# Performance work log

Measured on AMD Instinct MI355X. Metric: run time of the kernel, lower is better.

## Reference

```python
import jax, jax.numpy as jnp
import numpy as np

B, T = 128, 2048
N_IN, N_H, N_OUT = 16, 128, 5
I_DECAY, V_DECAY = 1024, 128          # Loihi 12-bit decay constants
ALPHA_I = (4096 - I_DECAY) / 4096.0   # current decay multiplier
ALPHA_V = (4096 - V_DECAY) / 4096.0   # voltage decay multiplier
W_SCALE = 64.0                        # Loihi synaptic weight scaling (1 << 6)
THETA = 1 * 64.0                      # vThMant * (1 << 6)
SCALE_RHO, TAU_RHO = 1.0, 1.0
SG_TAU = TAU_RHO * THETA              # surrogate-gradient width


@jax.custom_vjp
def spike_fn(x):
    # Heaviside spike with SLAYER exponential surrogate gradient
    return (x >= 0).astype(x.dtype)

def _spike_fwd(x):
    return spike_fn(x), x

def _spike_bwd(x, g):
    return (g * (SCALE_RHO / SG_TAU) * jnp.exp(-jnp.abs(x) / SG_TAU),)

spike_fn.defvjp(_spike_fwd, _spike_bwd)


def weight_norm(v, g):
    # torch weight_norm with dim=0: per-output-row normalization
    return g[:, None] * v / jnp.linalg.norm(v, axis=1, keepdims=True)


def loihi_spikes(z):
    # z: (B, O, T) synaptic input. Sequential Loihi CUBA integrate-and-fire.
    zt = jnp.transpose(z, (2, 0, 1))  # (T, B, O)

    def step(carry, zin):
        u, v = carry
        u = ALPHA_I * u + zin          # synaptic current
        v = ALPHA_V * v + u            # membrane voltage
        s = spike_fn(v - THETA)
        v = v * (1.0 - s)              # reset-to-zero on spike
        return (u, v), s

    init = (jnp.zeros(zt.shape[1:], zt.dtype), jnp.zeros(zt.shape[1:], zt.dtype))
    _, s = jax.lax.scan(step, init, zt)
    return jnp.transpose(s, (1, 2, 0))  # (B, O, T)


def delay_shift1(x):
    # shift spikes one timestep later (slayer.delayShift(spike, 1))
    return jnp.concatenate([jnp.zeros_like(x[..., :1]), x[..., :-1]], axis=-1)


def axon_delay(x, d):
    # per-channel fractional delay via linear interpolation; x: (B,C,T), d: (C,)
    Tn = x.shape[-1]
    d0 = jnp.floor(d)
    f = (d - d0)[None, :, None]
    d0i = d0.astype(jnp.int32)
    t = jnp.arange(Tn, dtype=jnp.int32)

    def gather(shift):
        idx = t[None, :] - shift[:, None]          # (C, T)
        g = jnp.take_along_axis(
            x, jnp.broadcast_to(jnp.clip(idx, 0, Tn - 1)[None], x.shape), axis=-1)
        return jnp.where((idx >= 0)[None], g, 0.0)

    return (1.0 - f) * gather(d0i) + f * gather(d0i + 1)


def setup_inputs() -> dict:
    key = jax.random.key(0)
    ks = jax.random.split(key, 8)
    spike = (jax.random.uniform(ks[0], (B, N_IN, T)) < 0.1).astype(jnp.float32)
    fc1_v = jax.random.normal(ks[1], (N_H, N_IN), jnp.float32)
    fc2_v = jax.random.normal(ks[2], (N_H, N_H), jnp.float32)
    fc3_v = jax.random.normal(ks[3], (N_OUT, N_H), jnp.float32)
    # weight_norm init: g = ||v|| so W == v initially
    fc1_g = jnp.linalg.norm(fc1_v, axis=1)
    fc2_g = jnp.linalg.norm(fc2_v, axis=1)
    fc3_g = jnp.linalg.norm(fc3_v, axis=1)
    delay1 = jax.random.uniform(ks[4], (N_H,), jnp.float32) * 10.0
    delay2 = jax.random.uniform(ks[5], (N_H,), jnp.float32) * 10.0
    return {"spike": spike, "fc1_v": fc1_v, "fc1_g": fc1_g, "fc2_v": fc2_v,
            "fc2_g": fc2_g, "fc3_v": fc3_v, "fc3_g": fc3_g,
            "delay1": delay1, "delay2": delay2}


def reference(spike, fc1_v, fc1_g, fc2_v, fc2_g, fc3_v, fc3_g, delay1, delay2):
    x = spike.reshape(spike.shape[0], -1, spike.shape[-1])  # (B, 16, T)
    counts = []

    s = loihi_spikes(W_SCALE * jnp.einsum('oc,bct->bot', weight_norm(fc1_v, fc1_g), x))
    s = delay_shift1(s)
    counts.append(jnp.sum(s))
    s = axon_delay(s, delay1)

    s = loihi_spikes(W_SCALE * jnp.einsum('oc,bct->bot', weight_norm(fc2_v, fc2_g), s))
    s = delay_shift1(s)
    counts.append(jnp.sum(s))
    s = axon_delay(s, delay2)

    s = loihi_spikes(W_SCALE * jnp.einsum('oc,bct->bot', weight_norm(fc3_v, fc3_g), s))
    s = delay_shift1(s)
    counts.append(jnp.sum(s))

    return s, jnp.stack(counts).reshape(1, 3)
```

## Files before the change

### kernel.cpp

```cpp
#include <hip/hip_runtime.h>
#include <cstdint>

#define B_    128
#define T_    2048
#define NIN_  16
#define NH_   128
#define NOUT_ 5

#define ALPHA_I_ 0.75f
#define ALPHA_V_ 0.96875f
#define THETA_   64.0f

#define NCHUNK_ 8
#define CHT_    256
#define WARM_   96

typedef short bf16x8 __attribute__((ext_vector_type(8)));
typedef float f32x16 __attribute__((ext_vector_type(16)));

__device__ __forceinline__ float mulrn(float a, float b) { return __fmul_rn(a, b); }
__device__ __forceinline__ float addrn(float a, float b) { return __fadd_rn(a, b); }

__device__ __forceinline__ uint16_t f2bf(float x) {
  uint32_t u = __float_as_uint(x);
  return (uint16_t)((u + 0x7FFFu + ((u >> 16) & 1u)) >> 16);
}

__device__ __forceinline__ bf16x8 expand8(const uint2* __restrict__ lut, uint32_t byt) {
  uint2 lo = lut[byt & 15u];
  uint2 h  = lut[byt >> 4];
  union { uint32_t w[4]; bf16x8 f; } r;
  r.w[0] = lo.x; r.w[1] = lo.y; r.w[2] = h.x; r.w[3] = h.y;
  return r.f;
}

__device__ __forceinline__ void lut_init(uint2* s_lut, int tid) {
  if (tid < 16) {
    uint32_t w0 = ((tid & 1) ? 0x3F80u : 0u) | ((tid & 2) ? 0x3F800000u : 0u);
    uint32_t w1 = ((tid & 4) ? 0x3F80u : 0u) | ((tid & 8) ? 0x3F800000u : 0u);
    s_lut[tid] = make_uint2(w0, w1);
  }
}

__global__ __launch_bounds__(1024) void prep_kernel(
    const float* __restrict__ fc1_v, const float* __restrict__ fc1_g,
    const float* __restrict__ fc2_v, const float* __restrict__ fc2_g,
    const float* __restrict__ fc3_v, const float* __restrict__ fc3_g,
    const float* __restrict__ delay1, const float* __restrict__ delay2,
    uint16_t* __restrict__ w1swz, uint16_t* __restrict__ wswz,
    float* __restrict__ w3T, float4* __restrict__ efo1, float4* __restrict__ efo2,
    float* __restrict__ counts) {
  __shared__ float s_n1[NH_], s_n2[NH_], s_n3[8], s_g2[NH_];
  int tid = threadIdx.x;
  {
    int o = tid >> 3, sub = tid & 7;
    float ss = 0.f;
    for (int c = sub; c < NIN_; c += 8) { float v = fc1_v[o * NIN_ + c]; ss = __fmaf_rn(v, v, ss); }
    ss += __shfl_down(ss, 4, 64); ss += __shfl_down(ss, 2, 64); ss += __shfl_down(ss, 1, 64);
    if (sub == 0) s_n1[o] = sqrtf(ss);
    float ss2 = 0.f;
    for (int c = sub; c < NH_; c += 8) { float v = fc2_v[o * NH_ + c]; ss2 = __fmaf_rn(v, v, ss2); }
    ss2 += __shfl_down(ss2, 4, 64); ss2 += __shfl_down(ss2, 2, 64); ss2 += __shfl_down(ss2, 1, 64);
    if (sub == 0) s_n2[o] = sqrtf(ss2);
  }
  if (tid < NOUT_ * 8) {
    int o = tid >> 3, sub = tid & 7;
    float ss = 0.f;
    for (int c = sub; c < NH_; c += 8) { float v = fc3_v[o * NH_ + c]; ss = __fmaf_rn(v, v, ss); }
    ss += __shfl_down(ss, 4, 64); ss += __shfl_down(ss, 2, 64); ss += __shfl_down(ss, 1, 64);
    if (sub == 0) s_n3[o] = sqrtf(ss);
  }
  if (tid < NH_) s_g2[tid] = fc2_g[tid];
  if (tid < 3) counts[tid] = 0.f;
  __syncthreads();

  if (tid < NH_) {
    float d1 = delay1[tid];
    float fl = floorf(d1);
    float f = __fsub_rn(d1, fl);
    efo1[tid] = make_float4(__int_as_float((int)fl + 1), f, __fsub_rn(1.0f, f), 0.f);
    float d2 = delay2[tid];
    float fl2 = floorf(d2);
    float f2v = __fsub_rn(d2, fl2);
    efo2[tid] = make_float4(__int_as_float((int)fl2 + 1), f2v, __fsub_rn(1.0f, f2v), 0.f);
    w3T[tid * 8 + 5] = f2v;
    w3T[tid * 8 + 6] = __fsub_rn(1.0f, f2v);
    w3T[tid * 8 + 7] = 0.f;
  }
  for (int i = tid; i < NH_ * NIN_; i += 1024) {
    int o = i >> 4, c = i & 15;
    float wv = 64.0f * __fdiv_rn(mulrn(fc1_g[o], fc1_v[i]), s_n1[o]);
    int mt = o >> 5, lane = (o & 31) + 32 * ((c >> 3) & 1), j = c & 7;
    w1swz[(mt * 64 + lane) * 8 + j] = f2bf(wv);
  }
  for (int i = tid; i < NH_ * NH_; i += 1024) {
    int o = i >> 7, c = i & 127;
    float wv = 64.0f * __fdiv_rn(mulrn(s_g2[o], fc2_v[i]), s_n2[o]);
    float d1 = delay1[c];
    float f = __fsub_rn(d1, floorf(d1));
    int lane = (o & 31) + 32 * ((c >> 3) & 1);
    int ks = c >> 4, j = c & 7, mt = o >> 5;
    wswz[((size_t)((0 * 4 + mt) * 8 + ks) * 64 + lane) * 8 + j] = f2bf(__fmul_rn(wv, f));
    wswz[((size_t)((1 * 4 + mt) * 8 + ks) * 64 + lane) * 8 + j] =
        f2bf(__fmul_rn(wv, __fsub_rn(1.0f, f)));
  }
  for (int i = tid; i < NOUT_ * NH_; i += 1024) {
    int o = i / NH_, c = i & 127;
    float wv = 64.0f * __fdiv_rn(mulrn(fc3_g[o], fc3_v[i]), s_n3[o]);
    w3T[c * 8 + o] = wv;
  }
}

__global__ __launch_bounds__(256) void pack_kernel(const float* __restrict__ spike,
                                                   uint16_t* __restrict__ Xb) {
  int gw = blockIdx.x * 4 + (threadIdx.x >> 6);
  int lane = threadIdx.x & 63;
  int b = gw >> 5;
  int t = (gw & 31) * 64 + lane;
  const float* sp = spike + (size_t)b * NIN_ * T_ + t;
  uint32_t mask = 0;
#pragma unroll
  for (int c = 0; c < NIN_; c++) {
    unsigned long long bal = __ballot(sp[(size_t)c * T_] != 0.f);
    mask |= (uint32_t)((bal >> lane) & 1ull) << c;
  }
  Xb[(size_t)b * T_ + t] = (uint16_t)mask;
}

#define GATHER_AND_SCAN(aA, aB, hi, u, v, m)                               \
  {                                                                        \
    float evenQ[16], oddQ[16];                                             \
    _Pragma("unroll") for (int r = 0; r < 16; r++) {                       \
      float tmp = hi ? aA[r] : aB[r];                                      \
      float rcv = __shfl_xor(tmp, 32, 64);                                 \
      evenQ[r] = hi ? rcv : aA[r];                                         \
      oddQ[r] = hi ? aB[r] : rcv;                                          \
    }                                                                      \
    m = 0u;                                                                \
    _Pragma("unroll") for (int t = 0; t < 32; t++) {                       \
      int q = t >> 2;                                                      \
      int base = 4 * (q >> 1) + (t & 3);                                   \
      float z = (q & 1) ? oddQ[base] : evenQ[base];                        \
      u = addrn(mulrn(ALPHA_I_, u), z);                                    \
      v = addrn(mulrn(ALPHA_V_, v), u);                                    \
      bool sbit = (v >= THETA_);                                           \
      v = sbit ? 0.f : v;                                                  \
      m |= sbit ? (1u << t) : 0u;                                          \
    }                                                                      \
  }

#define EMIT_PT(m, m_prev, e_o, ptw, chwstart)                             \
  {                                                                        \
    uint32_t sm = (uint32_t)((((uint64_t)(m) << 32) | (m_prev)) >> (32 - (e_o))); \
    uint32_t myword = 0u;                                                  \
    _Pragma("unroll") for (int j = 0; j < 32; j++) {                       \
      unsigned long long bal_ = __ballot(((sm >> j) & 1u) != 0u);          \
      uint32_t w_ = hi ? (uint32_t)(bal_ >> 32) : (uint32_t)bal_;          \
      myword = (tl == j) ? w_ : myword;                                    \
    }                                                                      \
    ptw[(size_t)(1 + (chwstart) + tl) * 4 + (pair * 2 + hi)] = myword;     \
  }

__global__ __launch_bounds__(128, 2) void fused_layer1(const uint16_t* __restrict__ Xb,
                                                       const uint16_t* __restrict__ w1swz,
                                                       const float4* __restrict__ efo,
                                                       uint32_t* __restrict__ PT1,
                                                       float* __restrict__ cnt) {
  __shared__ uint2 s_lut[16];
  int tid = threadIdx.x;
  int pair = tid >> 6, lane = tid & 63;
  int hi = lane >> 5, tl = lane & 31;
  int ci = blockIdx.x, b = blockIdx.y;
  lut_init(s_lut, tid);
  const bf16x8* w1v = (const bf16x8*)w1swz;
  bf16x8 wA = w1v[(pair * 2 + 0) * 64 + lane];
  bf16x8 wB = w1v[(pair * 2 + 1) * 64 + lane];
  int e_o = __float_as_int(efo[tid].x);
  __syncthreads();

  int wch = (ci == 0) ? 0 : (WARM_ / 32);
  int nch = CHT_ / 32 + wch;
  int chbase0 = ci * CHT_ - wch * 32;
  const uint16_t* xb = Xb + (size_t)b * T_;
  uint32_t* ptw = PT1 + (size_t)b * (T_ + 1) * 4;

  float u = 0.f, v = 0.f, csum = 0.f;
  uint32_t m_prev = 0u;
  uint32_t x = xb[chbase0 + tl];
  for (int g = 0; g < nch; g++) {
    uint32_t xn = (g + 1 < nch) ? (uint32_t)xb[chbase0 + (g + 1) * 32 + tl] : 0u;
    uint32_t byt = (x >> (8 * hi)) & 0xFFu;
    bf16x8 e = expand8(s_lut, byt);
    f32x16 aA, aB;
#pragma unroll
    for (int r = 0; r < 16; r++) { aA[r] = 0.f; aB[r] = 0.f; }
    aA = __builtin_amdgcn_mfma_f32_32x32x16_bf16(e, wA, aA, 0, 0, 0);
    aB = __builtin_amdgcn_mfma_f32_32x32x16_bf16(e, wB, aB, 0, 0, 0);
    uint32_t m;
    GATHER_AND_SCAN(aA, aB, hi, u, v, m);
    if (g >= wch) {
      int chwstart = chbase0 + g * 32;
      EMIT_PT(m, m_prev, e_o, ptw, chwstart);
      int gw = chwstart >> 5;
      int pc = __popc(m);
      if (gw == 63) pc -= (int)(m >> 31);
      csum += (float)pc;
    }
    m_prev = m;
    x = xn;
  }
  if (ci == 0 && tid < 4) ptw[tid] = 0u;
  for (int off = 32; off; off >>= 1) csum += __shfl_down(csum, off, 64);
  if (lane == 0) atomicAdd(cnt, csum);
}

__global__ __launch_bounds__(128, 2) void fused_layer2(const uint32_t* __restrict__ PT1,
                                                       const uint16_t* __restrict__ wswz,
                                                       const float4* __restrict__ efo,
                                                       uint32_t* __restrict__ PT2,
                                                       float* __restrict__ cnt) {
  __shared__ uint2 s_lut[16];
  int tid = threadIdx.x;
  int pair = tid >> 6, lane = tid & 63;
  int hi = lane >> 5, tl = lane & 31;
  int ci = blockIdx.x, b = blockIdx.y;
  lut_init(s_lut, tid);
  const bf16x8* wsv = (const bf16x8*)wswz;
  int mtA = pair * 2, mtB = pair * 2 + 1;
  bf16x8 wfA[8], woA[8], wfB[8], woB[8];
#pragma unroll
  for (int ks = 0; ks < 8; ks++) {
    wfA[ks] = wsv[((size_t)((0 * 4 + mtA) * 8 + ks) * 64) + lane];
    woA[ks] = wsv[((size_t)((1 * 4 + mtA) * 8 + ks) * 64) + lane];
    wfB[ks] = wsv[((size_t)((0 * 4 + mtB) * 8 + ks) * 64) + lane];
    woB[ks] = wsv[((size_t)((1 * 4 + mtB) * 8 + ks) * 64) + lane];
  }
  int e_o = __float_as_int(efo[tid].x);
  __syncthreads();

  int wch = (ci == 0) ? 0 : (WARM_ / 32);
  int nch = CHT_ / 32 + wch;
  int chbase0 = ci * CHT_ - wch * 32;
  const uint4* pt = (const uint4*)PT1 + (size_t)b * (T_ + 1);
  uint32_t* ptw = PT2 + (size_t)b * (T_ + 1) * 4;

  float u = 0.f, v = 0.f, csum = 0.f;
  uint32_t m_prev = 0u;
  uint4 R0 = pt[chbase0 + tl];
  uint4 R1 = pt[chbase0 + tl + 1];
  for (int g = 0; g < nch; g++) {
    uint4 R0n = R0, R1n = R1;
    if (g + 1 < nch) {
      R0n = pt[chbase0 + (g + 1) * 32 + tl];
      R1n = pt[chbase0 + (g + 1) * 32 + tl + 1];
    }
    uint32_t r0w[4] = {R0.x, R0.y, R0.z, R0.w};
    uint32_t r1w[4] = {R1.x, R1.y, R1.z, R1.w};
    f32x16 aA, aB;
#pragma unroll
    for (int r = 0; r < 16; r++) { aA[r] = 0.f; aB[r] = 0.f; }
#pragma unroll
    for (int ks = 0; ks < 8; ks++) {
      int sh = 16 * (ks & 1) + 8 * hi;
      uint32_t b0 = (r0w[ks >> 1] >> sh) & 0xFFu;
      uint32_t b1 = (r1w[ks >> 1] >> sh) & 0xFFu;
      bf16x8 e0 = expand8(s_lut, b0);
      bf16x8 e1 = expand8(s_lut, b1);
      aA = __builtin_amdgcn_mfma_f32_32x32x16_bf16(e0, wfA[ks], aA, 0, 0, 0);
      aA = __builtin_amdgcn_mfma_f32_32x32x16_bf16(e1, woA[ks], aA, 0, 0, 0);
      aB = __builtin_amdgcn_mfma_f32_32x32x16_bf16(e0, wfB[ks], aB, 0, 0, 0);
      aB = __builtin_amdgcn_mfma_f32_32x32x16_bf16(e1, woB[ks], aB, 0, 0, 0);
    }
    uint32_t m;
    GATHER_AND_SCAN(aA, aB, hi, u, v, m);
    if (g >= wch) {
      int chwstart = chbase0 + g * 32;
      EMIT_PT(m, m_prev, e_o, ptw, chwstart);
      int gw = chwstart >> 5;
      int pc = __popc(m);
      if (gw == 63) pc -= (int)(m >> 31);
      csum += (float)pc;
    }
    m_prev = m;
    R0 = R0n; R1 = R1n;
  }
  if (ci == 0 && tid < 4) ptw[tid] = 0u;
  for (int off = 32; off; off >>= 1) csum += __shfl_down(csum, off, 64);
  if (lane == 0) atomicAdd(cnt, csum);
}

__global__ __launch_bounds__(256) void gemm3_kernel(const uint32_t* __restrict__ PTpad,
                                                    const float* __restrict__ w3T,
                                                    float* __restrict__ z) {
  int tid = threadIdx.x;
  int t = blockIdx.x * 256 + tid;
  int b = blockIdx.y;
  const uint4* pt = (const uint4*)PTpad + (size_t)b * (T_ + 1);
  uint4 R0 = pt[t];
  uint4 R1 = pt[t + 1];
  uint32_t r0w[4] = {R0.x, R0.y, R0.z, R0.w};
  uint32_t r1w[4] = {R1.x, R1.y, R1.z, R1.w};

  float acc[NOUT_];
#pragma unroll
  for (int o = 0; o < NOUT_; o++) acc[o] = 0.f;

#pragma unroll
  for (int c = 0; c < NH_; c++) {
    const float* wc = w3T + (c << 3);
    float f = wc[5], omf = wc[6];
    float fb0 = (float)((r0w[c >> 5] >> (c & 31)) & 1u);
    float fb1 = (float)((r1w[c >> 5] >> (c & 31)) & 1u);
    float val = __fmaf_rn(omf, fb1, __fmul_rn(f, fb0));
#pragma unroll
    for (int o = 0; o < NOUT_; o++) acc[o] = __fmaf_rn(wc[o], val, acc[o]);
  }

#pragma unroll
  for (int o = 0; o < NOUT_; o++)
    z[((size_t)b * NOUT_ + o) * T_ + t] = acc[o];
}

__global__ __launch_bounds__(256) void scan3_kernel(const float* __restrict__ z3,
                                                    float* __restrict__ out,
                                                    float* __restrict__ cnt) {
  int id = blockIdx.x * 256 + threadIdx.x;
  int row = id % (B_ * NOUT_);
  int ci = id / (B_ * NOUT_);
  int tstart = ci * CHT_;
  int t0 = (ci == 0) ? 0 : tstart - WARM_;
  const float4* zp4 = (const float4*)(z3 + (size_t)row * T_);

  float u = 0.f, v = 0.f, carry = 0.f;
  int cnt_i = 0;
  for (int gg = t0 / 16; gg < tstart / 16; gg++) {
#pragma unroll
    for (int q = 0; q < 4; q++) {
      float4 cv = zp4[gg * 4 + q];
      float zv[4] = {cv.x, cv.y, cv.z, cv.w};
#pragma unroll
      for (int j = 0; j < 4; j++) {
        u = addrn(mulrn(ALPHA_I_, u), zv[j]);
        v = addrn(mulrn(ALPHA_V_, v), u);
        bool s = (v >= THETA_);
        v = s ? 0.f : v;
        carry = s ? 1.f : 0.f;
      }
    }
  }
  float4* op4 = (float4*)(out + (size_t)row * T_ + tstart);
  for (int gg = 0; gg < CHT_ / 16; gg++) {
    float sarr[16];
#pragma unroll
    for (int q = 0; q < 4; q++) {
      float4 cv = zp4[(tstart / 16 + gg) * 4 + q];
      float zv[4] = {cv.x, cv.y, cv.z, cv.w};
#pragma unroll
      for (int j = 0; j < 4; j++) {
        u = addrn(mulrn(ALPHA_I_, u), zv[j]);
        v = addrn(mulrn(ALPHA_V_, v), u);
        bool s = (v >= THETA_);
        v = s ? 0.f : v;
        sarr[q * 4 + j] = s ? 1.f : 0.f;
      }
    }
#pragma unroll
    for (int k = 0; k < 16; k++) {
      int t = tstart + gg * 16 + k;
      if (t < T_ - 1) cnt_i += (sarr[k] != 0.f) ? 1 : 0;
    }
    op4[gg * 4 + 0] = make_float4(carry, sarr[0], sarr[1], sarr[2]);
    op4[gg * 4 + 1] = make_float4(sarr[3], sarr[4], sarr[5], sarr[6]);
    op4[gg * 4 + 2] = make_float4(sarr[7], sarr[8], sarr[9], sarr[10]);
    op4[gg * 4 + 3] = make_float4(sarr[11], sarr[12], sarr[13], sarr[14]);
    carry = sarr[15];
  }
  float c = (float)cnt_i;
  for (int off = 32; off; off >>= 1) c += __shfl_down(c, off, 64);
  if ((threadIdx.x & 63) == 0) atomicAdd(cnt, c);
}

extern "C" void kernel_launch(void* const* d_in, const int* in_sizes, int n_in,
                              void* d_out, int out_size, void* d_ws, size_t ws_size,
                              hipStream_t stream) {
  (void)in_sizes; (void)n_in; (void)out_size; (void)ws_size;
  const float* spike  = (const float*)d_in[0];
  const float* fc1_v  = (const float*)d_in[1];
  const float* fc1_g  = (const float*)d_in[2];
  const float* fc2_v  = (const float*)d_in[3];
  const float* fc2_g  = (const float*)d_in[4];
  const float* fc3_v  = (const float*)d_in[5];
  const float* fc3_g  = (const float*)d_in[6];
  const float* delay1 = (const float*)d_in[7];
  const float* delay2 = (const float*)d_in[8];
  float* out = (float*)d_out;

  float* ws = (float*)d_ws;
  float* w3T       = ws;
  float4* efo1     = (float4*)(ws + 1024);
  float4* efo2     = (float4*)(ws + 1536);
  uint16_t* w1swz  = (uint16_t*)(ws + 2048);
  uint16_t* wswz   = (uint16_t*)(ws + 3072);
  uint16_t* Xb     = (uint16_t*)(ws + 19456);
  uint32_t* PT1    = (uint32_t*)(ws + 150528);
  uint32_t* PT2    = (uint32_t*)(ws + 1264640);
  float* z3        = ws + 2313728;
  float* counts = out + (size_t)B_ * NOUT_ * T_;

  prep_kernel<<<1, 1024, 0, stream>>>(fc1_v, fc1_g, fc2_v, fc2_g, fc3_v, fc3_g,
                                      delay1, delay2, w1swz, wswz, w3T, efo1, efo2, counts);

  pack_kernel<<<dim3(B_ * T_ / 64 / 4), 256, 0, stream>>>(spike, Xb);

  fused_layer1<<<dim3(NCHUNK_, B_), 128, 0, stream>>>(Xb, w1swz, efo1, PT1, counts + 0);

  fused_layer2<<<dim3(NCHUNK_, B_), 128, 0, stream>>>(PT1, wswz, efo2, PT2, counts + 1);

  gemm3_kernel<<<dim3(T_ / 256, B_), 256, 0, stream>>>(PT2, w3T, z3);
  scan3_kernel<<<dim3(NCHUNK_ * B_ * NOUT_ / 256), 256, 0, stream>>>(z3, out, counts + 2);
}
```

Measured before the change: 222.6 us.

## Fuse layer-3 GEMM and Loihi scan into one kernel via LDS

Merges the layer-3 projection kernel and the chunked scan kernel into a single kernel per (chunk, batch) block. Each block computes the synaptic input for its chunk plus the warmup window into shared memory, then 5 threads run the sequential scan from LDS. This removes the z3 global round trip and one launch. In exchange it recomputes the GEMM over the warmup region and runs the scan on only 5 lanes per block, which leaves the rest of the block idle during that phase.

New measurement: 239.9 us. 1.08x slower.

```diff
diff --git a/kernel.cpp b/kernel.cpp
--- a/kernel.cpp
+++ b/kernel.cpp
@@ -289,95 +289,88 @@
   if (lane == 0) atomicAdd(cnt, csum);
 }
 
-__global__ __launch_bounds__(256) void gemm3_kernel(const uint32_t* __restrict__ PTpad,
-                                                    const float* __restrict__ w3T,
-                                                    float* __restrict__ z) {
+__global__ __launch_bounds__(256) void tail_kernel(const uint32_t* __restrict__ PTpad,
+                                                   const float* __restrict__ w3T,
+                                                   float* __restrict__ out,
+                                                   float* __restrict__ cnt) {
+  __shared__ float z_lds[NOUT_][CHT_ + WARM_ + 8];
   int tid = threadIdx.x;
-  int t = blockIdx.x * 256 + tid;
-  int b = blockIdx.y;
+  int ci = blockIdx.x, b = blockIdx.y;
+  int wsk = (ci == 0) ? 0 : WARM_;
+  int nt = CHT_ + wsk;
+  int t0 = ci * CHT_ - wsk;
   const uint4* pt = (const uint4*)PTpad + (size_t)b * (T_ + 1);
-  uint4 R0 = pt[t];
-  uint4 R1 = pt[t + 1];
-  uint32_t r0w[4] = {R0.x, R0.y, R0.z, R0.w};
-  uint32_t r1w[4] = {R1.x, R1.y, R1.z, R1.w};
-
-  float acc[NOUT_];
-#pragma unroll
-  for (int o = 0; o < NOUT_; o++) acc[o] = 0.f;
-
-#pragma unroll
-  for (int c = 0; c < NH_; c++) {
-    const float* wc = w3T + (c << 3);
-    float f = wc[5], omf = wc[6];
-    float fb0 = (float)((r0w[c >> 5] >> (c & 31)) & 1u);
-    float fb1 = (float)((r1w[c >> 5] >> (c & 31)) & 1u);
-    float val = __fmaf_rn(omf, fb1, __fmul_rn(f, fb0));
-#pragma unroll
-    for (int o = 0; o < NOUT_; o++) acc[o] = __fmaf_rn(wc[o], val, acc[o]);
-  }
-
-#pragma unroll
-  for (int o = 0; o < NOUT_; o++)
-    z[((size_t)b * NOUT_ + o) * T_ + t] = acc[o];
-}
-
-__global__ __launch_bounds__(256) void scan3_kernel(const float* __restrict__ z3,
-                                                    float* __restrict__ out,
-                                                    float* __restrict__ cnt) {
-  int id = blockIdx.x * 256 + threadIdx.x;
-  int row = id % (B_ * NOUT_);
-  int ci = id / (B_ * NOUT_);
-  int tstart = ci * CHT_;
-  int t0 = (ci == 0) ? 0 : tstart - WARM_;
-  const float4* zp4 = (const float4*)(z3 + (size_t)row * T_);
-
-  float u = 0.f, v = 0.f, carry = 0.f;
-  int cnt_i = 0;
-  for (int gg = t0 / 16; gg < tstart / 16; gg++) {
-#pragma unroll
-    for (int q = 0; q < 4; q++) {
-      float4 cv = zp4[gg * 4 + q];
-      float zv[4] = {cv.x, cv.y, cv.z, cv.w};
-#pragma unroll
-      for (int j = 0; j < 4; j++) {
-        u = addrn(mulrn(ALPHA_I_, u), zv[j]);
+
+  for (int tt = tid; tt < nt; tt += 256) {
+    int t = t0 + tt;
+    uint4 R0 = pt[t];
+    uint4 R1 = pt[t + 1];
+    uint32_t r0w[4] = {R0.x, R0.y, R0.z, R0.w};
+    uint32_t r1w[4] = {R1.x, R1.y, R1.z, R1.w};
+    float acc[NOUT_];
+#pragma unroll
+    for (int o = 0; o < NOUT_; o++) acc[o] = 0.f;
+#pragma unroll
+    for (int c = 0; c < NH_; c++) {
+      const float* wc = w3T + (c << 3);
+      float f = wc[5], omf = wc[6];
+      float fb0 = (float)((r0w[c >> 5] >> (c & 31)) & 1u);
+      float fb1 = (float)((r1w[c >> 5] >> (c & 31)) & 1u);
+      float val = __fmaf_rn(omf, fb1, __fmul_rn(f, fb0));
+#pragma unroll
+      for (int o = 0; o < NOUT_; o++) acc[o] = __fmaf_rn(wc[o], val, acc[o]);
+    }
+#pragma unroll
+    for (int o = 0; o < NOUT_; o++) z_lds[o][tt] = acc[o];
+  }
+  __syncthreads();
+
+  if (tid < 64) {
+    int o = tid;
+    float csum = 0.f;
+    if (o < NOUT_) {
+      float u = 0.f, v = 0.f, carry = 0.f;
+      int cnt_i = 0;
+      int tstart = ci * CHT_;
+#pragma unroll 8
+      for (int tt = 0; tt < wsk; tt++) {
+        float z = z_lds[o][tt];
+        u = addrn(mulrn(ALPHA_I_, u), z);
         v = addrn(mulrn(ALPHA_V_, v), u);
         bool s = (v >= THETA_);
         v = s ? 0.f : v;
         carry = s ? 1.f : 0.f;
       }
-    }
-  }
-  float4* op4 = (float4*)(out + (size_t)row * T_ + tstart);
-  for (int gg = 0; gg < CHT_ / 16; gg++) {
-    float sarr[16];
-#pragma unroll
-    for (int q = 0; q < 4; q++) {
-      float4 cv = zp4[(tstart / 16 + gg) * 4 + q];
-      float zv[4] = {cv.x, cv.y, cv.z, cv.w};
-#pragma unroll
-      for (int j = 0; j < 4; j++) {
-        u = addrn(mulrn(ALPHA_I_, u), zv[j]);
-        v = addrn(mulrn(ALPHA_V_, v), u);
-        bool s = (v >= THETA_);
-        v = s ? 0.f : v;
-        sarr[q * 4 + j] = s ? 1.f : 0.f;
+      float4* op4 = (float4*)(out + ((size_t)b * NOUT_ + o) * T_ + tstart);
+      for (int gg = 0; gg < CHT_ / 16; gg++) {
+        float sarr[16];
+#pragma unroll
+        for (int k = 0; k < 16; k++) {
+          float z = z_lds[o][wsk + gg * 16 + k];
+          u = addrn(mulrn(ALPHA_I_, u), z);
+          v = addrn(mulrn(ALPHA_V_, v), u);
+          bool s = (v >= THETA_);
+          v = s ? 0.f : v;
+          sarr[k] = s ? 1.f : 0.f;
+        }
+#pragma unroll
+        for (int k = 0; k < 16; k++) {
+          int t = tstart + gg * 16 + k;
+          if (t < T_ - 1) cnt_i += (sarr[k] != 0.f) ? 1 : 0;
+        }
+        op4[gg * 4 + 0] = make_float4(carry, sarr[0], sarr[1], sarr[2]);
+        op4[gg * 4 + 1] = make_float4(sarr[3], sarr[4], sarr[5], sarr[6]);
+        op4[gg * 4 + 2] = make_float4(sarr[7], sarr[8], sarr[9], sarr[10]);
+        op4[gg * 4 + 3] = make_float4(sarr[11], sarr[12], sarr[13], sarr[14]);
+        carry = sarr[15];
       }
-    }
-#pragma unroll
-    for (int k = 0; k < 16; k++) {
-      int t = tstart + gg * 16 + k;
-      if (t < T_ - 1) cnt_i += (sarr[k] != 0.f) ? 1 : 0;
-    }
-    op4[gg * 4 + 0] = make_float4(carry, sarr[0], sarr[1], sarr[2]);
-    op4[gg * 4 + 1] = make_float4(sarr[3], sarr[4], sarr[5], sarr[6]);
-    op4[gg * 4 + 2] = make_float4(sarr[7], sarr[8], sarr[9], sarr[10]);
-    op4[gg * 4 + 3] = make_float4(sarr[11], sarr[12], sarr[13], sarr[14]);
-    carry = sarr[15];
-  }
-  float c = (float)cnt_i;
-  for (int off = 32; off; off >>= 1) c += __shfl_down(c, off, 64);
-  if ((threadIdx.x & 63) == 0) atomicAdd(cnt, c);
+      csum = (float)cnt_i;
+    }
+    csum += __shfl_down(csum, 4, 64);
+    csum += __shfl_down(csum, 2, 64);
+    csum += __shfl_down(csum, 1, 64);
+    if (tid == 0) atomicAdd(cnt, csum);
+  }
 }
 
 extern "C" void kernel_launch(void* const* d_in, const int* in_sizes, int n_in,
@@ -404,7 +397,6 @@
   uint16_t* Xb     = (uint16_t*)(ws + 19456);
   uint32_t* PT1    = (uint32_t*)(ws + 150528);
   uint32_t* PT2    = (uint32_t*)(ws + 1264640);
-  float* z3        = ws + 2313728;
   float* counts = out + (size_t)B_ * NOUT_ * T_;
 
   prep_kernel<<<1, 1024, 0, stream>>>(fc1_v, fc1_g, fc2_v, fc2_g, fc3_v, fc3_g,
@@ -416,6 +408,5 @@
 
   fused_layer2<<<dim3(NCHUNK_, B_), 128, 0, stream>>>(PT1, wswz, efo2, PT2, counts + 1);
 
-  gemm3_kernel<<<dim3(T_ / 256, B_), 256, 0, stream>>>(PT2, w3T, z3);
-  scan3_kernel<<<dim3(NCHUNK_ * B_ * NOUT_ / 256), 256, 0, stream>>>(z3, out, counts + 2);
-}
+  tail_kernel<<<dim3(NCHUNK_, B_), 256, 0, stream>>>(PT2, w3T, out, counts + 2);
+}
```
